# Kernel tuning notes

Measured on AMD Instinct MI355X. Metric: run time of the kernel, lower is better.

## Reference

```python
import jax, jax.numpy as jnp
import numpy as np

D = 1024        # model dim (== moe_inter_dim, required by Expert's x2*x3)
H = 1024        # expert hidden dim (moe_inter_dim)
E = 8           # n_routed_experts
K = 2           # n_activated_experts (top-k)
I = 2 * 1024    # shared-expert inter dim = n_shared_experts * moe_inter_dim
ROUTE_SCALE = 1.0


def setup_inputs() -> dict:
    key = jax.random.key(0)
    ks = jax.random.split(key, 12)
    s = lambda *sh: 1.0 / np.sqrt(sh[-1])
    return {
        "x":      jax.random.normal(ks[0], (1, 2048, D), jnp.float32),
        "gate_w": jax.random.normal(ks[1], (E, D), jnp.float32) * s(E, D),
        "w1":     jax.random.normal(ks[2], (E, H, D), jnp.float32) * s(H, D),
        "b1":     jax.random.normal(ks[3], (E, H), jnp.float32) * 0.01,
        "w2":     jax.random.normal(ks[4], (E, D, H), jnp.float32) * s(D, H),
        "b2":     jax.random.normal(ks[5], (E, D), jnp.float32) * 0.01,
        "w3":     jax.random.normal(ks[6], (E, H, D), jnp.float32) * s(H, D),
        "b3":     jax.random.normal(ks[7], (E, H), jnp.float32) * 0.01,
        "sw1":    jax.random.normal(ks[8], (I, D), jnp.float32) * s(I, D),
        "sw2":    jax.random.normal(ks[9], (I, D), jnp.float32) * s(I, D),
        "sw3":    jax.random.normal(ks[10], (D, I), jnp.float32) * s(D, I),
    }


def reference(x, gate_w, w1, b1, w2, b2, w3, b3, sw1, sw2, sw3):
    B, S, _ = x.shape
    xt = x.reshape(-1, D)                                  # (T, D)
    # ---- Gate (softmax scoring, n_groups==1, no bias, route_scale=1) ----
    logits = xt @ gate_w.T                                 # (T, E)
    scores = jax.nn.softmax(logits.astype(jnp.float32), axis=-1)
    top_vals, idx = jax.lax.top_k(scores, K)               # (T, K)
    weights = (jnp.take_along_axis(scores, idx, axis=1)
               .astype(x.dtype)) * ROUTE_SCALE             # (T, K)
    # ---- Routed experts: input is scaled by routing weight BEFORE expert ----
    xs = xt[:, None, :] * weights[:, :, None]              # (T, K, D)
    y = jnp.zeros_like(xt)
    for e in range(E):  # fixed small loop over experts (dense masked dispatch)
        mask = (idx == e).astype(x.dtype)                  # (T, K)
        h = jax.nn.silu(jnp.einsum('tkd,hd->tkh', xs, w1[e]) + b1[e])
        x2 = jnp.einsum('tkh,dh->tkd', h, w2[e]) + b2[e]   # (T, K, D)
        x3 = jnp.einsum('tkd,hd->tkh', xs, w3[e]) + b3[e]  # (T, K, H==D)
        y = y + jnp.sum((x2 * x3) * mask[:, :, None], axis=1)
    # ---- Shared experts (SwiGLU MLP, no biases) ----
    z = (jax.nn.silu(xt @ sw1.T) * (xt @ sw2.T)) @ sw3.T   # (T, D)
    return (y + z).reshape(B, S, D)
```

## Files before the change

### kernel.cpp

```cpp
#include <hip/hip_runtime.h>

typedef unsigned short u16;
typedef __attribute__((ext_vector_type(4))) float floatx4;
typedef __attribute__((ext_vector_type(8))) short short8;

#define MAXROWS 5120
#define MAXMT 40

__device__ __forceinline__ u16 f2bf(float f) {
    union { float f; unsigned u; } v; v.f = f;
    unsigned r = v.u + 0x7FFF + ((v.u >> 16) & 1);
    return (u16)(r >> 16);
}
__device__ __forceinline__ float bf2f(u16 h) {
    union { unsigned u; float f; } v; v.u = ((unsigned)h) << 16; return v.f;
}
__device__ __forceinline__ float silu_f(float x) { return x / (1.f + __expf(-x)); }

__device__ __forceinline__ void gl_lds16(const void* g, void* l) {
    __builtin_amdgcn_global_load_lds(
        (__attribute__((address_space(1))) unsigned int*)g,
        (__attribute__((address_space(3))) unsigned int*)l, 16, 0, 0);
}

__global__ void conv_gate(const float* __restrict__ w1, const float* __restrict__ w2,
                          const float* __restrict__ w3, const float* __restrict__ sw1,
                          const float* __restrict__ sw2, const float* __restrict__ sw3,
                          const float* __restrict__ x, const float* __restrict__ gw,
                          u16* __restrict__ W13, u16* __restrict__ W2b,
                          u16* __restrict__ S12, u16* __restrict__ S3b,
                          u16* __restrict__ Xb,
                          int* __restrict__ idxA, float* __restrict__ wA) {
    int bid = blockIdx.x;
    if (bid < 512) {
        int w = threadIdx.x >> 6, lane = threadIdx.x & 63;
        int t = bid * 4 + w;
        const float* xr = x + (size_t)t * 1024;
        float acc[8];
#pragma unroll
        for (int e = 0; e < 8; e++) acc[e] = 0.f;
#pragma unroll
        for (int i = 0; i < 16; i++) {
            float xv = xr[lane + (i << 6)];
#pragma unroll
            for (int e = 0; e < 8; e++) acc[e] += xv * gw[e * 1024 + lane + (i << 6)];
        }
#pragma unroll
        for (int e = 0; e < 8; e++)
            for (int off = 32; off > 0; off >>= 1) acc[e] += __shfl_xor(acc[e], off);
        if (lane == 0) {
            float m = acc[0];
#pragma unroll
            for (int e = 1; e < 8; e++) m = fmaxf(m, acc[e]);
            float p[8], s = 0.f;
#pragma unroll
            for (int e = 0; e < 8; e++) { p[e] = __expf(acc[e] - m); s += p[e]; }
            float inv = 1.f / s;
#pragma unroll
            for (int e = 0; e < 8; e++) p[e] *= inv;
            int i0 = 0;
#pragma unroll
            for (int e = 1; e < 8; e++) if (p[e] > p[i0]) i0 = e;
            int i1 = (i0 == 0) ? 1 : 0;
            for (int e = i1 + 1; e < 8; e++) if (e != i0 && p[e] > p[i1]) i1 = e;
            idxA[2 * t] = i0; idxA[2 * t + 1] = i1;
            wA[2 * t] = p[i0]; wA[2 * t + 1] = p[i1];
        }
        return;
    }
    long j = (long)(bid - 512) * 256 + threadIdx.x;
    const float* src; u16* dst; long d;
    if (j < 2097152) {
        long e = j >> 18; src = w1; dst = W13; d = j + (e << 18);
    } else if ((j -= 2097152) < 2097152) {
        long e = j >> 18; src = w3; dst = W13; d = j + (e << 18) + 262144;
    } else if ((j -= 2097152) < 2097152) { src = w2;  dst = W2b; d = j; }
    else if ((j -= 2097152) < 524288) {
        long rr = j >> 8, c4 = j & 255;
        long br = ((rr >> 4) << 5) + (rr & 15);
        src = sw1; dst = S12; d = (br << 8) + c4;
    } else if ((j -= 524288) < 524288) {
        long rr = j >> 8, c4 = j & 255;
        long br = ((rr >> 4) << 5) + 16 + (rr & 15);
        src = sw2; dst = S12; d = (br << 8) + c4;
    } else if ((j -= 524288) < 524288)     { src = sw3; dst = S3b; d = j; }
    else { j -= 524288; src = x; dst = Xb; d = j; }
    float4 v = ((const float4*)src)[j];
    ushort4 o; o.x = f2bf(v.x); o.y = f2bf(v.y); o.z = f2bf(v.z); o.w = f2bf(v.w);
    ((ushort4*)dst)[d] = o;
}

__global__ void rank_k(const int* __restrict__ idxA, int* __restrict__ tileexp,
                       int* __restrict__ ntiles, int* __restrict__ slot_of) {
    int lane = threadIdx.x;
    const int* my = idxA + lane * 64;
    int h[8];
#pragma unroll
    for (int e = 0; e < 8; e++) h[e] = 0;
    for (int i = 0; i < 64; i++) {
        int v = my[i];
#pragma unroll
        for (int e = 0; e < 8; e++) h[e] += (v == e);
    }
    int excl[8], tot[8];
#pragma unroll
    for (int e = 0; e < 8; e++) {
        int inc = h[e];
        for (int off = 1; off < 64; off <<= 1) {
            int up = __shfl_up(inc, off);
            if (lane >= off) inc += up;
        }
        excl[e] = inc - h[e];
        tot[e] = __shfl(inc, 63);
    }
    int base[8], tiles = 0;
#pragma unroll
    for (int e = 0; e < 8; e++) {
        base[e] = tiles * 128;
        tiles += (tot[e] + 127) >> 7;
    }
    if (lane == 0) {
        ntiles[0] = tiles;
        int t = 0;
        for (int e = 0; e < 8; e++) {
            int te = (tot[e] + 127) >> 7;
            for (int j = 0; j < te; j++) tileexp[t++] = e;
        }
    }
    int c[8];
#pragma unroll
    for (int e = 0; e < 8; e++) c[e] = base[e] + excl[e];
    for (int i = 0; i < 64; i++) {
        int v = my[i], slot = 0;
#pragma unroll
        for (int e = 0; e < 8; e++) slot += (v == e) ? c[e] : 0;
#pragma unroll
        for (int e = 0; e < 8; e++) c[e] += (v == e);
        slot_of[lane * 64 + i] = slot;
    }
}

__global__ void build_xs(const float* __restrict__ x, const float* __restrict__ wA,
                         const int* __restrict__ slot_of, u16* __restrict__ XS) {
    int s = blockIdx.x, i = threadIdx.x;
    int t = s >> 1; float w = wA[s]; int slot = slot_of[s];
    float4 v = ((const float4*)(x + (size_t)t * 1024))[i];
    ushort4 o; o.x = f2bf(v.x * w); o.y = f2bf(v.y * w); o.z = f2bf(v.z * w); o.w = f2bf(v.w * w);
    ((ushort4*)(XS + (size_t)slot * 1024))[i] = o;
}

__global__ __launch_bounds__(256) void gemm_A(
    const u16* __restrict__ XS, const u16* __restrict__ Xb,
    const u16* __restrict__ W13, const u16* __restrict__ S12,
    const float* __restrict__ b1, const float* __restrict__ b3,
    u16* __restrict__ H, u16* __restrict__ X3h, u16* __restrict__ G,
    const int* __restrict__ tileexp, const int* __restrict__ ntiles) {
    __shared__ u16 ldsA[128 * 32];
    __shared__ u16 ldsB[128 * 32];
    int seg = blockIdx.x;
    const u16 *Ab, *Bb; int mt, nt, e = 0; bool routed;
    if (seg < 640) {
        routed = true; mt = seg % 40; nt = seg / 40;
        if (mt >= ntiles[0]) return;
        e = tileexp[mt];
        Ab = XS; Bb = W13 + ((size_t)e << 21);
    } else {
        routed = false; int s = seg - 640; mt = s & 15; nt = s >> 4;
        Ab = Xb; Bb = S12;
    }
    int m0 = mt * 128, n0 = nt * 128;
    int tid = threadIdx.x, w = tid >> 6, lane = tid & 63;
    int wm = w >> 1, wn = w & 1;

    floatx4 acc[4][4];
#pragma unroll
    for (int i = 0; i < 4; i++)
#pragma unroll
        for (int j = 0; j < 4; j++) { floatx4 z = {0.f, 0.f, 0.f, 0.f}; acc[i][j] = z; }

    int rloc = lane >> 2, clds = lane & 3, q = lane >> 4, l15 = lane & 15;

    for (int k0 = 0; k0 < 1024; k0 += 32) {
#pragma unroll
        for (int t = 0; t < 2; t++) {
            int r = (w << 4) + (t << 6) + rloc;
            int cg = clds ^ ((r >> 1) & 3);
            gl_lds16(Ab + (size_t)(m0 + r) * 1024 + k0 + (cg << 3),
                     &ldsA[((w << 4) + (t << 6)) * 32]);
            gl_lds16(Bb + (size_t)(n0 + r) * 1024 + k0 + (cg << 3),
                     &ldsB[((w << 4) + (t << 6)) * 32]);
        }
        __syncthreads();
        short8 af[4], bf[4];
#pragma unroll
        for (int i = 0; i < 4; i++) {
            int rr = (wm << 6) + (i << 4) + l15;
            int c = q ^ ((rr >> 1) & 3);
            af[i] = *(const short8*)&ldsA[rr * 32 + (c << 3)];
        }
#pragma unroll
        for (int j = 0; j < 4; j++) {
            int rr = (wn << 6) + (j << 4) + l15;
            int c = q ^ ((rr >> 1) & 3);
            bf[j] = *(const short8*)&ldsB[rr * 32 + (c << 3)];
        }
#pragma unroll
        for (int i = 0; i < 4; i++)
#pragma unroll
            for (int j = 0; j < 4; j++)
                acc[i][j] = __builtin_amdgcn_mfma_f32_16x16x32_bf16(af[i], bf[j], acc[i][j], 0, 0, 0);
        __syncthreads();
    }

    if (routed) {
#pragma unroll
        for (int i = 0; i < 4; i++) {
            int rowb = m0 + (wm << 6) + (i << 4) + (q << 2);
#pragma unroll
            for (int j = 0; j < 4; j++) {
                int col = n0 + (wn << 6) + (j << 4) + l15;
#pragma unroll
                for (int r = 0; r < 4; r++) {
                    float v = acc[i][j][r];
                    int rw = rowb + r;
                    if (nt < 8) {
                        H[(size_t)rw * 1024 + col] = f2bf(silu_f(v + b1[e * 1024 + col]));
                    } else {
                        int c2 = col - 1024;
                        X3h[(size_t)rw * 1024 + c2] = f2bf(v + b3[e * 1024 + c2]);
                    }
                }
            }
        }
    } else {
#pragma unroll
        for (int i = 0; i < 4; i++) {
            int rowb = m0 + (wm << 6) + (i << 4) + (q << 2);
#pragma unroll
            for (int jp = 0; jp < 4; jp += 2) {
                int brb = n0 + (wn << 6) + (jp << 4);
                int lcol = ((brb >> 5) << 4) + l15;
#pragma unroll
                for (int r = 0; r < 4; r++) {
                    float u = acc[i][jp][r], v = acc[i][jp + 1][r];
                    G[(size_t)(rowb + r) * 2048 + lcol] = f2bf(silu_f(u) * v);
                }
            }
        }
    }
}

__global__ __launch_bounds__(256) void gemm_B(
    const u16* __restrict__ H, const u16* __restrict__ G,
    const u16* __restrict__ W2b, const u16* __restrict__ S3b,
    const float* __restrict__ b2, const u16* __restrict__ X3h,
    u16* __restrict__ P0, u16* __restrict__ P1,
    float* __restrict__ Z0, float* __restrict__ Z1,
    const int* __restrict__ tileexp, const int* __restrict__ ntiles) {
    __shared__ u16 ldsA[128 * 32];
    __shared__ u16 ldsB[128 * 32];
    int seg = blockIdx.x;
    const u16 *Ab, *Bb; int mt, nt, kc, lda, kbeg, e = 0; bool routed;
    if (seg < 640) {
        routed = true; kc = seg & 1; int s2 = seg >> 1;
        mt = s2 % 40; nt = s2 / 40;
        if (mt >= ntiles[0]) return;
        e = tileexp[mt];
        Ab = H; Bb = W2b + ((size_t)e << 20); lda = 1024; kbeg = kc << 9;
    } else {
        routed = false; int s = seg - 640; kc = s & 1; int s2 = s >> 1;
        mt = s2 & 15; nt = s2 >> 4;
        Ab = G; Bb = S3b; lda = 2048; kbeg = kc << 10;
    }
    int kend = kbeg + (routed ? 512 : 1024);
    int m0 = mt * 128, n0 = nt * 128;
    int tid = threadIdx.x, w = tid >> 6, lane = tid & 63;
    int wm = w >> 1, wn = w & 1;

    floatx4 acc[4][4];
#pragma unroll
    for (int i = 0; i < 4; i++)
#pragma unroll
        for (int j = 0; j < 4; j++) { floatx4 z = {0.f, 0.f, 0.f, 0.f}; acc[i][j] = z; }

    int rloc = lane >> 2, clds = lane & 3, q = lane >> 4, l15 = lane & 15;

    for (int k0 = kbeg; k0 < kend; k0 += 32) {
#pragma unroll
        for (int t = 0; t < 2; t++) {
            int r = (w << 4) + (t << 6) + rloc;
            int cg = clds ^ ((r >> 1) & 3);
            gl_lds16(Ab + (size_t)(m0 + r) * lda + k0 + (cg << 3),
                     &ldsA[((w << 4) + (t << 6)) * 32]);
            gl_lds16(Bb + (size_t)(n0 + r) * lda + k0 + (cg << 3),
                     &ldsB[((w << 4) + (t << 6)) * 32]);
        }
        __syncthreads();
        short8 af[4], bf[4];
#pragma unroll
        for (int i = 0; i < 4; i++) {
            int rr = (wm << 6) + (i << 4) + l15;
            int c = q ^ ((rr >> 1) & 3);
            af[i] = *(const short8*)&ldsA[rr * 32 + (c << 3)];
        }
#pragma unroll
        for (int j = 0; j < 4; j++) {
            int rr = (wn << 6) + (j << 4) + l15;
            int c = q ^ ((rr >> 1) & 3);
            bf[j] = *(const short8*)&ldsB[rr * 32 + (c << 3)];
        }
#pragma unroll
        for (int i = 0; i < 4; i++)
#pragma unroll
            for (int j = 0; j < 4; j++)
                acc[i][j] = __builtin_amdgcn_mfma_f32_16x16x32_bf16(af[i], bf[j], acc[i][j], 0, 0, 0);
        __syncthreads();
    }

    if (routed) {
        u16* Pk = kc ? P1 : P0;
#pragma unroll
        for (int i = 0; i < 4; i++) {
            int rowb = m0 + (wm << 6) + (i << 4) + (q << 2);
#pragma unroll
            for (int j = 0; j < 4; j++) {
                int col = n0 + (wn << 6) + (j << 4) + l15;
#pragma unroll
                for (int r = 0; r < 4; r++) {
                    int rw = rowb + r;
                    float v = acc[i][j][r] + (kc == 0 ? b2[e * 1024 + col] : 0.f);
                    float pv = v * bf2f(X3h[(size_t)rw * 1024 + col]);
                    Pk[(size_t)rw * 1024 + col] = f2bf(pv);
                }
            }
        }
    } else {
        float* Zk = kc ? Z1 : Z0;
#pragma unroll
        for (int i = 0; i < 4; i++) {
            int rowb = m0 + (wm << 6) + (i << 4) + (q << 2);
#pragma unroll
            for (int j = 0; j < 4; j++) {
                int col = n0 + (wn << 6) + (j << 4) + l15;
#pragma unroll
                for (int r = 0; r < 4; r++)
                    Zk[(size_t)(rowb + r) * 1024 + col] = acc[i][j][r];
            }
        }
    }
}

__global__ void final_k(const float* __restrict__ Z0, const float* __restrict__ Z1,
                        const u16* __restrict__ P0, const u16* __restrict__ P1,
                        const int* __restrict__ slot_of, float* __restrict__ out) {
    int i = blockIdx.x * 256 + threadIdx.x;
    int t = i >> 8, c4 = i & 255;
    int s0 = slot_of[2 * t], s1 = slot_of[2 * t + 1];
    float4 z0 = ((const float4*)Z0)[(size_t)t * 256 + c4];
    float4 z1 = ((const float4*)Z1)[(size_t)t * 256 + c4];
    ushort4 a0 = ((const ushort4*)P0)[(size_t)s0 * 256 + c4];
    ushort4 a1 = ((const ushort4*)P1)[(size_t)s0 * 256 + c4];
    ushort4 c0 = ((const ushort4*)P0)[(size_t)s1 * 256 + c4];
    ushort4 c1 = ((const ushort4*)P1)[(size_t)s1 * 256 + c4];
    float4 o;
    o.x = z0.x + z1.x + bf2f(a0.x) + bf2f(a1.x) + bf2f(c0.x) + bf2f(c1.x);
    o.y = z0.y + z1.y + bf2f(a0.y) + bf2f(a1.y) + bf2f(c0.y) + bf2f(c1.y);
    o.z = z0.z + z1.z + bf2f(a0.z) + bf2f(a1.z) + bf2f(c0.z) + bf2f(c1.z);
    o.w = z0.w + z1.w + bf2f(a0.w) + bf2f(a1.w) + bf2f(c0.w) + bf2f(c1.w);
    ((float4*)out)[(size_t)t * 256 + c4] = o;
}

extern "C" void kernel_launch(void* const* d_in, const int* in_sizes, int n_in,
                              void* d_out, int out_size, void* d_ws, size_t ws_size,
                              hipStream_t stream) {
    const float* x   = (const float*)d_in[0];
    const float* gw  = (const float*)d_in[1];
    const float* w1  = (const float*)d_in[2];
    const float* b1  = (const float*)d_in[3];
    const float* w2  = (const float*)d_in[4];
    const float* b2  = (const float*)d_in[5];
    const float* w3  = (const float*)d_in[6];
    const float* b3  = (const float*)d_in[7];
    const float* sw1 = (const float*)d_in[8];
    const float* sw2 = (const float*)d_in[9];
    const float* sw3 = (const float*)d_in[10];
    float* out = (float*)d_out;

    char* p = (char*)d_ws;
    int* ntiles  = (int*)(p + 192);
    int* tileexp = (int*)(p + 256);
    size_t off = 4096;
    u16*   XS      = (u16*)(p + off);   off += (size_t)MAXROWS * 1024 * 2;
    int*   idxA    = (int*)(p + off);   off += 16384;
    float* wA      = (float*)(p + off); off += 16384;
    int*   slot_of = (int*)(p + off);   off += 16384;
    u16*   H       = (u16*)(p + off);   off += (size_t)MAXROWS * 1024 * 2;
    u16*   X3h     = (u16*)(p + off);   off += (size_t)MAXROWS * 1024 * 2;
    u16*   P0      = (u16*)(p + off);   off += (size_t)MAXROWS * 1024 * 2;
    u16*   P1      = (u16*)(p + off);   off += (size_t)MAXROWS * 1024 * 2;
    float* Z0      = (float*)(p + off); off += (size_t)2048 * 1024 * 4;
    float* Z1      = (float*)(p + off); off += (size_t)2048 * 1024 * 4;
    u16*   W13     = (u16*)(p + off);   off += (size_t)8 * 2048 * 1024 * 2;
    u16*   W2b     = (u16*)(p + off);   off += (size_t)8 * 1024 * 1024 * 2;
    u16*   S12     = (u16*)(p + off);   off += (size_t)4096 * 1024 * 2;
    u16*   S3b     = (u16*)(p + off);   off += (size_t)1024 * 2048 * 2;
    u16*   Xb      = (u16*)(p + off);   off += (size_t)2048 * 1024 * 2;
    u16*   G       = (u16*)(p + off);   off += (size_t)2048 * 2048 * 2;

    conv_gate<<<33280, 256, 0, stream>>>(w1, w2, w3, sw1, sw2, sw3, x, gw,
                                         W13, W2b, S12, S3b, Xb, idxA, wA);
    rank_k<<<1, 64, 0, stream>>>(idxA, tileexp, ntiles, slot_of);
    build_xs<<<4096, 256, 0, stream>>>(x, wA, slot_of, XS);

    gemm_A<<<1152, 256, 0, stream>>>(XS, Xb, W13, S12, b1, b3, H, X3h, G,
                                     tileexp, ntiles);
    gemm_B<<<896, 256, 0, stream>>>(H, G, W2b, S3b, b2, X3h, P0, P1, Z0, Z1,
                                    tileexp, ntiles);
    final_k<<<2048, 256, 0, stream>>>(Z0, Z1, P0, P1, slot_of, out);
}
```

Measured before the change: 334.0 us.

## Double K-step per barrier to 64 and pair N-tiles in block ordering

Both GEMM kernels now stage a 64-wide K slice (two 32-wide halves) into LDS per iteration instead of 32, halving the number of __syncthreads pairs and load/compute phase switches. LDS per block doubles to 32 KB. gemm_A also remaps block indices so that consecutive blocks cover two adjacent N tiles across all M tiles, which is meant to improve L2 reuse of the weight tiles. The larger LDS footprint may reduce occupancy.

```diff
diff --git a/kernel.cpp b/kernel.cpp
--- a/kernel.cpp
+++ b/kernel.cpp
@@ -149,23 +149,72 @@
     ((ushort4*)(XS + (size_t)slot * 1024))[i] = o;
 }
 
+#define STAGE64(Ab, Bb, lda)                                                        \
+    {                                                                               \
+        _Pragma("unroll")                                                           \
+        for (int t = 0; t < 2; t++) {                                               \
+            int b = w + (t << 2);                                                   \
+            int r = (b << 4) + rloc;                                                \
+            int cg = clds ^ ((r >> 1) & 3);                                         \
+            _Pragma("unroll")                                                       \
+            for (int hh = 0; hh < 2; hh++) {                                        \
+                gl_lds16(Ab + (size_t)(m0 + r) * lda + k0 + (hh << 5) + (cg << 3),  \
+                         &ldsA[(b * 2 + hh) * 512]);                                \
+                gl_lds16(Bb + (size_t)(n0 + r) * lda + k0 + (hh << 5) + (cg << 3),  \
+                         &ldsB[(b * 2 + hh) * 512]);                                \
+            }                                                                       \
+        }                                                                           \
+    }
+
+#define MFMA64()                                                                    \
+    {                                                                               \
+        _Pragma("unroll")                                                           \
+        for (int hh = 0; hh < 2; hh++) {                                            \
+            short8 af[4], bf[4];                                                    \
+            _Pragma("unroll")                                                       \
+            for (int i = 0; i < 4; i++) {                                           \
+                int rr = (wm << 6) + (i << 4) + l15;                                \
+                int g = q ^ ((rr >> 1) & 3);                                        \
+                af[i] = *(const short8*)&ldsA[((rr >> 4) * 2 + hh) * 512 +          \
+                                              (rr & 15) * 32 + (g << 3)];           \
+            }                                                                       \
+            _Pragma("unroll")                                                       \
+            for (int j = 0; j < 4; j++) {                                           \
+                int rr = (wn << 6) + (j << 4) + l15;                                \
+                int g = q ^ ((rr >> 1) & 3);                                        \
+                bf[j] = *(const short8*)&ldsB[((rr >> 4) * 2 + hh) * 512 +          \
+                                              (rr & 15) * 32 + (g << 3)];           \
+            }                                                                       \
+            _Pragma("unroll")                                                       \
+            for (int i = 0; i < 4; i++)                                             \
+                _Pragma("unroll")                                                   \
+                for (int j = 0; j < 4; j++)                                         \
+                    acc[i][j] = __builtin_amdgcn_mfma_f32_16x16x32_bf16(            \
+                        af[i], bf[j], acc[i][j], 0, 0, 0);                          \
+        }                                                                           \
+    }
+
 __global__ __launch_bounds__(256) void gemm_A(
     const u16* __restrict__ XS, const u16* __restrict__ Xb,
     const u16* __restrict__ W13, const u16* __restrict__ S12,
     const float* __restrict__ b1, const float* __restrict__ b3,
     u16* __restrict__ H, u16* __restrict__ X3h, u16* __restrict__ G,
     const int* __restrict__ tileexp, const int* __restrict__ ntiles) {
-    __shared__ u16 ldsA[128 * 32];
-    __shared__ u16 ldsB[128 * 32];
+    __shared__ u16 ldsA[128 * 64];
+    __shared__ u16 ldsB[128 * 64];
     int seg = blockIdx.x;
     const u16 *Ab, *Bb; int mt, nt, e = 0; bool routed;
     if (seg < 640) {
-        routed = true; mt = seg % 40; nt = seg / 40;
+        routed = true;
+        int pair = seg / 80, w80 = seg % 80;
+        mt = w80 % 40; nt = pair * 2 + w80 / 40;
         if (mt >= ntiles[0]) return;
         e = tileexp[mt];
         Ab = XS; Bb = W13 + ((size_t)e << 21);
     } else {
-        routed = false; int s = seg - 640; mt = s & 15; nt = s >> 4;
+        routed = false; int s = seg - 640;
+        int pair = s / 32, w32 = s % 32;
+        mt = w32 % 16; nt = pair * 2 + w32 / 16;
         Ab = Xb; Bb = S12;
     }
     int m0 = mt * 128, n0 = nt * 128;
@@ -180,35 +229,10 @@
 
     int rloc = lane >> 2, clds = lane & 3, q = lane >> 4, l15 = lane & 15;
 
-    for (int k0 = 0; k0 < 1024; k0 += 32) {
-#pragma unroll
-        for (int t = 0; t < 2; t++) {
-            int r = (w << 4) + (t << 6) + rloc;
-            int cg = clds ^ ((r >> 1) & 3);
-            gl_lds16(Ab + (size_t)(m0 + r) * 1024 + k0 + (cg << 3),
-                     &ldsA[((w << 4) + (t << 6)) * 32]);
-            gl_lds16(Bb + (size_t)(n0 + r) * 1024 + k0 + (cg << 3),
-                     &ldsB[((w << 4) + (t << 6)) * 32]);
-        }
+    for (int k0 = 0; k0 < 1024; k0 += 64) {
+        STAGE64(Ab, Bb, 1024);
         __syncthreads();
-        short8 af[4], bf[4];
-#pragma unroll
-        for (int i = 0; i < 4; i++) {
-            int rr = (wm << 6) + (i << 4) + l15;
-            int c = q ^ ((rr >> 1) & 3);
-            af[i] = *(const short8*)&ldsA[rr * 32 + (c << 3)];
-        }
-#pragma unroll
-        for (int j = 0; j < 4; j++) {
-            int rr = (wn << 6) + (j << 4) + l15;
-            int c = q ^ ((rr >> 1) & 3);
-            bf[j] = *(const short8*)&ldsB[rr * 32 + (c << 3)];
-        }
-#pragma unroll
-        for (int i = 0; i < 4; i++)
-#pragma unroll
-            for (int j = 0; j < 4; j++)
-                acc[i][j] = __builtin_amdgcn_mfma_f32_16x16x32_bf16(af[i], bf[j], acc[i][j], 0, 0, 0);
+        MFMA64();
         __syncthreads();
     }
 
@@ -257,22 +281,22 @@
     u16* __restrict__ P0, u16* __restrict__ P1,
     float* __restrict__ Z0, float* __restrict__ Z1,
     const int* __restrict__ tileexp, const int* __restrict__ ntiles) {
-    __shared__ u16 ldsA[128 * 32];
-    __shared__ u16 ldsB[128 * 32];
+    __shared__ u16 ldsA[128 * 64];
+    __shared__ u16 ldsB[128 * 64];
     int seg = blockIdx.x;
-    const u16 *Ab, *Bb; int mt, nt, kc, lda, kbeg, e = 0; bool routed;
+    const u16 *Ab, *Bb; int mt, nt, kc, lda, kbeg, kspan, e = 0; bool routed;
     if (seg < 640) {
         routed = true; kc = seg & 1; int s2 = seg >> 1;
         mt = s2 % 40; nt = s2 / 40;
         if (mt >= ntiles[0]) return;
         e = tileexp[mt];
-        Ab = H; Bb = W2b + ((size_t)e << 20); lda = 1024; kbeg = kc << 9;
+        Ab = H; Bb = W2b + ((size_t)e << 20); lda = 1024; kbeg = kc << 9; kspan = 512;
     } else {
         routed = false; int s = seg - 640; kc = s & 1; int s2 = s >> 1;
         mt = s2 & 15; nt = s2 >> 4;
-        Ab = G; Bb = S3b; lda = 2048; kbeg = kc << 10;
-    }
-    int kend = kbeg + (routed ? 512 : 1024);
+        Ab = G; Bb = S3b; lda = 2048; kbeg = kc << 10; kspan = 1024;
+    }
+    int kend = kbeg + kspan;
     int m0 = mt * 128, n0 = nt * 128;
     int tid = threadIdx.x, w = tid >> 6, lane = tid & 63;
     int wm = w >> 1, wn = w & 1;
@@ -285,35 +309,10 @@
 
     int rloc = lane >> 2, clds = lane & 3, q = lane >> 4, l15 = lane & 15;
 
-    for (int k0 = kbeg; k0 < kend; k0 += 32) {
-#pragma unroll
-        for (int t = 0; t < 2; t++) {
-            int r = (w << 4) + (t << 6) + rloc;
-            int cg = clds ^ ((r >> 1) & 3);
-            gl_lds16(Ab + (size_t)(m0 + r) * lda + k0 + (cg << 3),
-                     &ldsA[((w << 4) + (t << 6)) * 32]);
-            gl_lds16(Bb + (size_t)(n0 + r) * lda + k0 + (cg << 3),
-                     &ldsB[((w << 4) + (t << 6)) * 32]);
-        }
+    for (int k0 = kbeg; k0 < kend; k0 += 64) {
+        STAGE64(Ab, Bb, lda);
         __syncthreads();
-        short8 af[4], bf[4];
-#pragma unroll
-        for (int i = 0; i < 4; i++) {
-            int rr = (wm << 6) + (i << 4) + l15;
-            int c = q ^ ((rr >> 1) & 3);
-            af[i] = *(const short8*)&ldsA[rr * 32 + (c << 3)];
-        }
-#pragma unroll
-        for (int j = 0; j < 4; j++) {
-            int rr = (wn << 6) + (j << 4) + l15;
-            int c = q ^ ((rr >> 1) & 3);
-            bf[j] = *(const short8*)&ldsB[rr * 32 + (c << 3)];
-        }
-#pragma unroll
-        for (int i = 0; i < 4; i++)
-#pragma unroll
-            for (int j = 0; j < 4; j++)
-                acc[i][j] = __builtin_amdgcn_mfma_f32_16x16x32_bf16(af[i], bf[j], acc[i][j], 0, 0, 0);
+        MFMA64();
         __syncthreads();
     }
 
```

New measurement: 322.4 us. 3.5% less time.
